# Kernel tuning notes

Measured on AMD Instinct MI355X. Metric: run time of the kernel, lower is better.

## Reference

```python
import jax, jax.numpy as jnp
import numpy as np


def _mixture_log_cdf(x, pi, mu, s):
    # x: (B, C, H, W); pi/mu/s: (B, K, C, H, W); logistic log-CDF = log_sigmoid(z)
    z = (x[:, None] - mu) * jnp.exp(-s)
    return jax.scipy.special.logsumexp(
        jax.nn.log_softmax(pi, axis=1) + jax.nn.log_sigmoid(z), axis=1)


def _mixture_log_pdf(x, pi, mu, s):
    # logistic log-pdf: -z - log_scale - 2*softplus(-z), z = (x - mu) / exp(s)
    z = (x[:, None] - mu) * jnp.exp(-s)
    log_pdf = -z - s - 2.0 * jax.nn.softplus(-z)
    return jax.scipy.special.logsumexp(
        jax.nn.log_softmax(pi, axis=1) + log_pdf, axis=1)


def setup_inputs() -> dict:
    key = jax.random.key(0)
    B, C, H, W, K = 16, 64, 64, 64, 16
    Ch = C // 2
    ks = jax.random.split(key, 6)
    return {
        'x': jax.random.normal(ks[0], (B, C, H, W), jnp.float32),
        'sldj': jnp.zeros((B,), jnp.float32),
        'a': jax.random.normal(ks[1], (B, Ch, H, W), jnp.float32),
        'b': jax.random.normal(ks[2], (B, Ch, H, W), jnp.float32),
        'pi': jax.random.normal(ks[3], (B, K, Ch, H, W), jnp.float32),
        'mu': jax.random.normal(ks[4], (B, K, Ch, H, W), jnp.float32),
        's': jax.random.normal(ks[5], (B, K, Ch, H, W), jnp.float32),
    }


def reference(x, sldj, a, b, pi, mu, s):
    C = x.shape[1]
    x_change, x_id = x[:, :C // 2], x[:, C // 2:]
    # forward direction (reverse=False)
    log_cdf = _mixture_log_cdf(x_change, pi, mu, s)   # (B, C/2, H, W)
    u = jnp.exp(log_cdf)
    # logistic.inverse: logit(u); ldj = -log(u) - log(1-u)
    out = jnp.log(u) - jnp.log1p(-u)
    scale_ldj = -jnp.log(u) - jnp.log1p(-u)
    out = (out + b) * jnp.exp(a)
    logistic_ldj = _mixture_log_pdf(x_change, pi, mu, s)
    sldj = sldj + (logistic_ldj + scale_ldj + a).reshape(x.shape[0], -1).sum(-1)
    return jnp.concatenate([out, x_id], axis=1), sldj
```

## Files before the change

kernel.cpp:

```cpp
#include <hip/hip_runtime.h>
#include <math.h>

constexpr int NB = 16, NK = 16, NCh = 32, NH = 64, NW = 64;
constexpr int HW = NH * NW;
constexpr int PER_BATCH = NCh * HW;
constexpr int NTOT = NB * PER_BATCH;
constexpr int PMS_BSTRIDE = NK * PER_BATCH;

__global__ void init_sldj_kernel(const float* __restrict__ sldj_in,
                                 float* __restrict__ out_sldj) {
    int i = threadIdx.x;
    if (i < NB) out_sldj[i] = sldj_in[i];
}

__launch_bounds__(256, 4)
__global__ void mixlogcdf_kernel(const float* __restrict__ x,
                                 const float* __restrict__ a,
                                 const float* __restrict__ b,
                                 const float* __restrict__ pi,
                                 const float* __restrict__ mu,
                                 const float* __restrict__ s,
                                 float* __restrict__ out,
                                 float* __restrict__ out_sldj) {
    const int tid   = blockIdx.x * 256 + threadIdx.x;
    const int gid   = tid << 2;
    const int batch = gid >> 17;
    const int rem   = gid & (PER_BATCH - 1);
    const int xbase = (batch << 18) | rem;

    const float4 x4 = *(const float4*)(x + xbase);
    const float4 a4 = *(const float4*)(a + gid);
    const float4 b4 = *(const float4*)(b + gid);
    const float xv[4] = {x4.x, x4.y, x4.z, x4.w};
    const float av[4] = {a4.x, a4.y, a4.z, a4.w};
    const float bv[4] = {b4.x, b4.y, b4.z, b4.w};

    const size_t base = (size_t)batch * PMS_BSTRIDE + rem;
    const float* pip = pi + base;
    const float* mup = mu + base;
    const float* skp = s + base;

    float sumw[4] = {0.f, 0.f, 0.f, 0.f};
    float scdf[4] = {0.f, 0.f, 0.f, 0.f};
    float sccdf[4] = {0.f, 0.f, 0.f, 0.f};
    float spdf[4] = {0.f, 0.f, 0.f, 0.f};

#pragma unroll
    for (int k = 0; k < NK; ++k) {
        const float4 p4 = *(const float4*)(pip + (size_t)k * PER_BATCH);
        const float4 m4 = *(const float4*)(mup + (size_t)k * PER_BATCH);
        const float4 s4 = *(const float4*)(skp + (size_t)k * PER_BATCH);
        const float pk[4] = {p4.x, p4.y, p4.z, p4.w};
        const float mk[4] = {m4.x, m4.y, m4.z, m4.w};
        const float sk[4] = {s4.x, s4.y, s4.z, s4.w};
#pragma unroll
        for (int e = 0; e < 4; ++e) {
            const float es = __expf(-sk[e]);
            float z = (xv[e] - mk[e]) * es;
            z = fmaxf(z, -87.0f);
            const float t   = __expf(-z);
            const float sig = __builtin_amdgcn_rcpf(1.0f + t);
            const float ep  = __expf(pk[e]);
            const float epc = ep * sig;
            const float cc  = epc * t;
            sumw[e] += ep;
            scdf[e] += epc;
            sccdf[e] += cc;
            spdf[e] = fmaf(cc, sig * es, spdf[e]);
        }
    }

    float4 o4;
    float* op = &o4.x;
    float srow = 0.f;
#pragma unroll
    for (int e = 0; e < 4; ++e) {
        const float lsp  = __logf(sumw[e]);
        const float lsc  = __logf(fmaxf(scdf[e], 1e-37f));
        const float lscc = __logf(fmaxf(sccdf[e], 1e-37f));
        const float lst  = __logf(fmaxf(spdf[e], 1e-37f));
        op[e] = (lsc - lscc + bv[e]) * __expf(av[e]);
        srow += lst + lsp - lsc - lscc + av[e];
    }
    *(float4*)(out + xbase) = o4;
    *(float4*)(out + xbase + PER_BATCH) = *(const float4*)(x + xbase + PER_BATCH);

#pragma unroll
    for (int off = 32; off > 0; off >>= 1) srow += __shfl_down(srow, off, 64);
    __shared__ float wsum[4];
    const int lane = threadIdx.x & 63;
    const int wid  = threadIdx.x >> 6;
    if (lane == 0) wsum[wid] = srow;
    __syncthreads();
    if (threadIdx.x == 0) {
        atomicAdd(&out_sldj[batch], wsum[0] + wsum[1] + wsum[2] + wsum[3]);
    }
}

extern "C" void kernel_launch(void* const* d_in, const int* in_sizes, int n_in,
                              void* d_out, int out_size, void* d_ws, size_t ws_size,
                              hipStream_t stream) {
    const float* x    = (const float*)d_in[0];
    const float* sldj = (const float*)d_in[1];
    const float* a    = (const float*)d_in[2];
    const float* b    = (const float*)d_in[3];
    const float* pi   = (const float*)d_in[4];
    const float* mu   = (const float*)d_in[5];
    const float* s    = (const float*)d_in[6];

    float* out      = (float*)d_out;
    float* out_sldj = out + (size_t)NB * 2 * PER_BATCH;

    init_sldj_kernel<<<1, 64, 0, stream>>>(sldj, out_sldj);
    mixlogcdf_kernel<<<NTOT / 1024, 256, 0, stream>>>(x, a, b, pi, mu, s, out, out_sldj);
}
```

Measured before the change: 102.3 us.

## Double-buffer mixture parameter loads with inline-asm global loads and explicit vmcnt waits

Replaces the per-k loop of compiler-scheduled float4 loads with a hand-pipelined scheme. Inline-asm global_load_dwordx4 fills two register buffers of four mixture components each for pi, mu and s, and s_waitcnt vmcnt plus sched barriers let compute on one buffer overlap loads into the other. The x, a, b and pass-through loads are also issued up front. The launch-bounds occupancy hint is dropped to leave room for the larger register footprint. The aim is more memory-level parallelism in this bandwidth-bound kernel, at the cost of fragile manual waitcnt bookkeeping that the compiler cannot check.

After: 93.10 us. -9.0%, faster.

```diff
diff --git a/kernel.cpp b/kernel.cpp
--- a/kernel.cpp
+++ b/kernel.cpp
@@ -1,5 +1,7 @@
 #include <hip/hip_runtime.h>
 #include <math.h>
+
+typedef float f32x4 __attribute__((ext_vector_type(4)));
 
 constexpr int NB = 16, NK = 16, NCh = 32, NH = 64, NW = 64;
 constexpr int HW = NH * NW;
@@ -13,7 +15,45 @@
     if (i < NB) out_sldj[i] = sldj_in[i];
 }
 
-__launch_bounds__(256, 4)
+#define GLOAD4(dst, addr) \
+    asm volatile("global_load_dwordx4 %0, %1, off" : "=v"(dst) : "v"(addr))
+
+#define VMWAIT(N)                                              \
+    do {                                                       \
+        asm volatile("s_waitcnt vmcnt(" #N ")" ::: "memory");  \
+        __builtin_amdgcn_sched_barrier(0);                     \
+    } while (0)
+
+#define ISSUE(buf, kbase)                                                     \
+    do {                                                                      \
+        _Pragma("unroll") for (int j = 0; j < 4; ++j) {                       \
+            GLOAD4(Pb[buf][j], pp + (size_t)((kbase) + j) * PER_BATCH);       \
+            GLOAD4(Mb[buf][j], mp + (size_t)((kbase) + j) * PER_BATCH);       \
+            GLOAD4(Sb[buf][j], sp + (size_t)((kbase) + j) * PER_BATCH);       \
+        }                                                                     \
+    } while (0)
+
+#define COMPUTE(buf)                                                          \
+    do {                                                                      \
+        _Pragma("unroll") for (int j = 0; j < 4; ++j) {                       \
+            _Pragma("unroll") for (int e = 0; e < 4; ++e) {                   \
+                const float es = __expf(-Sb[buf][j][e]);                      \
+                float z = (x4[e] - Mb[buf][j][e]) * es;                       \
+                z = fmaxf(z, -87.0f);                \
+                const float t   = __expf(-z);                                 \
+                const float sig = __builtin_amdgcn_rcpf(1.0f + t);            \
+                const float ep  = __expf(Pb[buf][j][e]);                      \
+                const float epc = ep * sig;                                   \
+                const float cc  = epc * t;                                    \
+                sumw[e]  += ep;                                               \
+                scdf[e]  += epc;                                              \
+                sccdf[e] += cc;                                               \
+                spdf[e]   = fmaf(cc, sig * es, spdf[e]);                      \
+            }                                                                 \
+        }                                                                     \
+    } while (0)
+
+__launch_bounds__(256)
 __global__ void mixlogcdf_kernel(const float* __restrict__ x,
                                  const float* __restrict__ a,
                                  const float* __restrict__ b,
@@ -28,50 +68,38 @@
     const int rem   = gid & (PER_BATCH - 1);
     const int xbase = (batch << 18) | rem;
 
-    const float4 x4 = *(const float4*)(x + xbase);
-    const float4 a4 = *(const float4*)(a + gid);
-    const float4 b4 = *(const float4*)(b + gid);
-    const float xv[4] = {x4.x, x4.y, x4.z, x4.w};
-    const float av[4] = {a4.x, a4.y, a4.z, a4.w};
-    const float bv[4] = {b4.x, b4.y, b4.z, b4.w};
+    const size_t base = (size_t)batch * PMS_BSTRIDE + rem;
+    const float* pp = pi + base;
+    const float* mp = mu + base;
+    const float* sp = s + base;
 
-    const size_t base = (size_t)batch * PMS_BSTRIDE + rem;
-    const float* pip = pi + base;
-    const float* mup = mu + base;
-    const float* skp = s + base;
+    f32x4 x4, a4, b4, id4;
+    GLOAD4(x4, x + xbase);
+    GLOAD4(a4, a + gid);
+    GLOAD4(b4, b + gid);
+    GLOAD4(id4, x + xbase + PER_BATCH);
 
-    float sumw[4] = {0.f, 0.f, 0.f, 0.f};
-    float scdf[4] = {0.f, 0.f, 0.f, 0.f};
+    f32x4 Pb[2][4], Mb[2][4], Sb[2][4];
+    ISSUE(0, 0);
+    ISSUE(1, 4);
+
+    float sumw[4]  = {0.f, 0.f, 0.f, 0.f};
+    float scdf[4]  = {0.f, 0.f, 0.f, 0.f};
     float sccdf[4] = {0.f, 0.f, 0.f, 0.f};
-    float spdf[4] = {0.f, 0.f, 0.f, 0.f};
+    float spdf[4]  = {0.f, 0.f, 0.f, 0.f};
 
-#pragma unroll
-    for (int k = 0; k < NK; ++k) {
-        const float4 p4 = *(const float4*)(pip + (size_t)k * PER_BATCH);
-        const float4 m4 = *(const float4*)(mup + (size_t)k * PER_BATCH);
-        const float4 s4 = *(const float4*)(skp + (size_t)k * PER_BATCH);
-        const float pk[4] = {p4.x, p4.y, p4.z, p4.w};
-        const float mk[4] = {m4.x, m4.y, m4.z, m4.w};
-        const float sk[4] = {s4.x, s4.y, s4.z, s4.w};
-#pragma unroll
-        for (int e = 0; e < 4; ++e) {
-            const float es = __expf(-sk[e]);
-            float z = (xv[e] - mk[e]) * es;
-            z = fmaxf(z, -87.0f);
-            const float t   = __expf(-z);
-            const float sig = __builtin_amdgcn_rcpf(1.0f + t);
-            const float ep  = __expf(pk[e]);
-            const float epc = ep * sig;
-            const float cc  = epc * t;
-            sumw[e] += ep;
-            scdf[e] += epc;
-            sccdf[e] += cc;
-            spdf[e] = fmaf(cc, sig * es, spdf[e]);
-        }
-    }
+    VMWAIT(12);
+    COMPUTE(0);
+    ISSUE(0, 8);
+    VMWAIT(12);
+    COMPUTE(1);
+    ISSUE(1, 12);
+    VMWAIT(12);
+    COMPUTE(0);
+    VMWAIT(0);
+    COMPUTE(1);
 
-    float4 o4;
-    float* op = &o4.x;
+    f32x4 o4;
     float srow = 0.f;
 #pragma unroll
     for (int e = 0; e < 4; ++e) {
@@ -79,11 +107,11 @@
         const float lsc  = __logf(fmaxf(scdf[e], 1e-37f));
         const float lscc = __logf(fmaxf(sccdf[e], 1e-37f));
         const float lst  = __logf(fmaxf(spdf[e], 1e-37f));
-        op[e] = (lsc - lscc + bv[e]) * __expf(av[e]);
-        srow += lst + lsp - lsc - lscc + av[e];
+        o4[e] = (lsc - lscc + b4[e]) * __expf(a4[e]);
+        srow += lst + lsp - lsc - lscc + a4[e];
     }
-    *(float4*)(out + xbase) = o4;
-    *(float4*)(out + xbase + PER_BATCH) = *(const float4*)(x + xbase + PER_BATCH);
+    *(f32x4*)(out + xbase) = o4;
+    *(f32x4*)(out + xbase + PER_BATCH) = id4;
 
 #pragma unroll
     for (int off = 32; off > 0; off >>= 1) srow += __shfl_down(srow, off, 64);
```
